# Performance work log

Hardware: AMD Instinct MI355X
Metric: run time of the kernel (lower is better)

## Reference

```python
import jax, jax.numpy as jnp
import numpy as np
from jax import lax


def setup_inputs() -> dict:
    key = jax.random.key(0)
    x = jax.random.normal(key, (8, 1, 2048, 2048), dtype=jnp.float32)
    return {"x": x}


def reference(x):
    # torch.median over the whole tensor returns the LOWER median for even counts:
    # k-th smallest element with k = (n - 1) // 2.
    n = x.size
    med = jnp.sort(x.ravel())[(n - 1) // 2]

    # Threshold everything <= median to zero.
    thr = jnp.where(x > med, x, jnp.zeros_like(x))

    # 7x7 max pool, stride 1, padding 3 (torch pads with -inf), output same HxW.
    maxed = lax.reduce_window(
        thr,
        -jnp.inf,
        lax.max,
        window_dimensions=(1, 1, 7, 7),
        window_strides=(1, 1, 1, 1),
        padding=((0, 0), (0, 0), (3, 3), (3, 3)),
    )

    # Keep only local maxima (entries equal to their window max), scaled by score.
    out = jnp.where(thr == maxed, thr, jnp.zeros_like(thr))
    return out
```

## Files before the change

kernel.cpp:

```cpp
#include <hip/hip_runtime.h>
#include <math.h>

#define IMG_H 2048
#define IMG_W 2048
#define TX 64
#define TY 64
#define HALO 3
#define IN_W (TX + 2 * HALO)
#define IN_H (TY + 2 * HALO)
#define SIN_STRIDE 71
#define SHM_STRIDE 65
#define CAND_CAP (1u << 20)
#define CBUF 1024

__device__ __forceinline__ unsigned f2key(unsigned u) {
    unsigned mask = (unsigned)(((int)u >> 31)) | 0x80000000u;
    return u ^ mask;
}
static inline unsigned f2key_host(float f) {
    union { float f; unsigned u; } c; c.f = f;
    unsigned mask = (unsigned)(((int)c.u >> 31)) | 0x80000000u;
    return c.u ^ mask;
}

__device__ __forceinline__ unsigned block_exscan(unsigned val, unsigned* tmp) {
    const int t = threadIdx.x;
    tmp[t] = val;
    __syncthreads();
#pragma unroll
    for (int off = 1; off < 256; off <<= 1) {
        unsigned v = (t >= off) ? tmp[t - off] : 0u;
        __syncthreads();
        tmp[t] += v;
        __syncthreads();
    }
    return tmp[t] - val;
}

template <int C>
__device__ __forceinline__ void find_crossing(const unsigned* bins, unsigned k,
                                              unsigned* tmp, unsigned* res) {
    unsigned s = 0;
#pragma unroll
    for (int j = 0; j < C; ++j) s += bins[threadIdx.x * C + j];
    unsigned ex = block_exscan(s, tmp);
    if (k >= ex && k < ex + s) {
        unsigned cum = ex;
        int b = threadIdx.x * C;
        while (cum + bins[b] <= k) { cum += bins[b]; ++b; }
        res[0] = (unsigned)b;
        res[1] = k - cum;
    }
    __syncthreads();
}

__global__ __launch_bounds__(256) void hist_window_kernel(
        const float4* __restrict__ x, int n4, unsigned* __restrict__ ghist,
        unsigned* __restrict__ ctrl, unsigned* __restrict__ candA,
        unsigned keyLo, unsigned keyHi) {
    __shared__ unsigned h[4 * 2048];
    __shared__ unsigned cbuf[CBUF];
    __shared__ unsigned ccnt, sbase, scnt;
    const int wave = threadIdx.x >> 6;
    unsigned* hw = &h[wave * 2048];
    for (int i = threadIdx.x; i < 4 * 2048; i += 256) h[i] = 0;
    if (threadIdx.x == 0) ccnt = 0;
    __syncthreads();
    const int stride = gridDim.x * blockDim.x;
    for (int i = blockIdx.x * blockDim.x + threadIdx.x; i < n4; i += stride) {
        float4 v = x[i];
        unsigned k0 = f2key(__float_as_uint(v.x));
        unsigned k1 = f2key(__float_as_uint(v.y));
        unsigned k2 = f2key(__float_as_uint(v.z));
        unsigned k3 = f2key(__float_as_uint(v.w));
        atomicAdd(&hw[k0 >> 21], 1u);
        atomicAdd(&hw[k1 >> 21], 1u);
        atomicAdd(&hw[k2 >> 21], 1u);
        atomicAdd(&hw[k3 >> 21], 1u);
        if (k0 > keyLo && k0 < keyHi) { unsigned p = atomicAdd(&ccnt, 1u); if (p < CBUF) cbuf[p] = k0; }
        if (k1 > keyLo && k1 < keyHi) { unsigned p = atomicAdd(&ccnt, 1u); if (p < CBUF) cbuf[p] = k1; }
        if (k2 > keyLo && k2 < keyHi) { unsigned p = atomicAdd(&ccnt, 1u); if (p < CBUF) cbuf[p] = k2; }
        if (k3 > keyLo && k3 < keyHi) { unsigned p = atomicAdd(&ccnt, 1u); if (p < CBUF) cbuf[p] = k3; }
    }
    __syncthreads();
    for (int b = threadIdx.x; b < 2048; b += 256) {
        unsigned s = h[b] + h[2048 + b] + h[4096 + b] + h[6144 + b];
        if (s) atomicAdd(&ghist[b], s);
    }
    if (threadIdx.x == 0) {
        unsigned c = ccnt;
        if (c > CBUF) { c = CBUF; atomicOr(&ctrl[3], 1u); }
        unsigned base = atomicAdd(&ctrl[2], c);
        if (base + c > CAND_CAP) {
            atomicOr(&ctrl[3], 1u);
            c = base < CAND_CAP ? CAND_CAP - base : 0;
        }
        sbase = base; scnt = c;
    }
    __syncthreads();
    for (unsigned i = threadIdx.x; i < scnt; i += 256) candA[sbase + i] = cbuf[i];
}

__global__ __launch_bounds__(256) void find_bucket_kernel(
        const unsigned* __restrict__ ghist, unsigned k, unsigned* __restrict__ ctrl,
        unsigned keyLo, unsigned keyHi) {
    __shared__ unsigned lh[2048];
    __shared__ unsigned tmp[256];
    __shared__ unsigned res[2];
    for (int i = threadIdx.x; i < 2048; i += 256) lh[i] = ghist[i];
    __syncthreads();
    find_crossing<8>(lh, k, tmp, res);
    if (threadIdx.x == 0) {
        unsigned b = res[0];
        ctrl[0] = b;
        ctrl[1] = res[1];
        unsigned lo = b << 21, hi = (b << 21) + 0x1FFFFFu;
        ctrl[4] = (lo > keyLo && hi < keyHi && ctrl[3] == 0u) ? 1u : 0u;
    }
}

__global__ __launch_bounds__(256) void compact_fallback_kernel(
        const float4* __restrict__ x, int n4, unsigned* __restrict__ ctrl,
        unsigned* __restrict__ candB) {
    if (ctrl[4]) return;
    const unsigned bucket = ctrl[0];
    const int stride = gridDim.x * blockDim.x;
    for (int i = blockIdx.x * blockDim.x + threadIdx.x; i < n4; i += stride) {
        float4 v = x[i];
        unsigned ks[4] = { f2key(__float_as_uint(v.x)), f2key(__float_as_uint(v.y)),
                           f2key(__float_as_uint(v.z)), f2key(__float_as_uint(v.w)) };
#pragma unroll
        for (int j = 0; j < 4; ++j)
            if ((ks[j] >> 21) == bucket) {
                unsigned p = atomicAdd(&ctrl[5], 1u);
                if (p < CAND_CAP) candB[p] = ks[j];
            }
    }
}

__global__ __launch_bounds__(256) void bucket_filter_kernel(
        const unsigned* __restrict__ ctrl_c, unsigned* __restrict__ ctrl,
        const unsigned* __restrict__ candA, unsigned* __restrict__ candC) {
    if (!ctrl_c[4]) return;
    const unsigned bucket = ctrl_c[0];
    unsigned M = ctrl_c[2];
    if (M > CAND_CAP) M = CAND_CAP;
    const int stride = gridDim.x * blockDim.x;
    for (unsigned i = blockIdx.x * blockDim.x + threadIdx.x; i < M; i += stride) {
        unsigned key = candA[i];
        if ((key >> 21) == bucket) {
            unsigned p = atomicAdd(&ctrl[6], 1u);
            if (p < CAND_CAP) candC[p] = key;
        }
    }
}

__global__ __launch_bounds__(256) void final_select_kernel(
        unsigned* __restrict__ ctrl, const unsigned* __restrict__ candC,
        const unsigned* __restrict__ candB, float* __restrict__ medp) {
    __shared__ unsigned h2[2048];
    __shared__ unsigned tmp[256];
    __shared__ unsigned res[2];
    const unsigned covered = ctrl[4];
    const unsigned* src = covered ? candC : candB;
    unsigned M = covered ? ctrl[6] : ctrl[5];
    if (M > CAND_CAP) M = CAND_CAP;
    const unsigned bucket = ctrl[0];
    const unsigned r = ctrl[1];

    for (int i = threadIdx.x; i < 2048; i += 256) h2[i] = 0;
    __syncthreads();
    for (unsigned i = threadIdx.x; i < M; i += 256) {
        unsigned key = src[i];
        if ((key >> 21) == bucket) atomicAdd(&h2[(key >> 10) & 0x7FFu], 1u);
    }
    __syncthreads();
    find_crossing<8>(h2, r, tmp, res);
    const unsigned pref = (bucket << 11) | res[0];
    const unsigned r2 = res[1];
    __syncthreads();

    for (int i = threadIdx.x; i < 1024; i += 256) h2[i] = 0;
    __syncthreads();
    for (unsigned i = threadIdx.x; i < M; i += 256) {
        unsigned key = src[i];
        if ((key >> 10) == pref) atomicAdd(&h2[key & 0x3FFu], 1u);
    }
    __syncthreads();
    find_crossing<4>(h2, r2, tmp, res);
    if (threadIdx.x == 0) {
        unsigned key = (pref << 10) | res[0];
        unsigned u = (key & 0x80000000u) ? (key ^ 0x80000000u) : ~key;
        *medp = __uint_as_float(u);
    }
}

__global__ __launch_bounds__(256) void nms_kernel(const float* __restrict__ x,
                                                  float* __restrict__ out,
                                                  const float* __restrict__ medp) {
    __shared__ float sin_[IN_H * SIN_STRIDE];
    __shared__ float shm[IN_H * SHM_STRIDE];
    const float med = *medp;
    const int tx0 = blockIdx.x * TX;
    const int ty0 = blockIdx.y * TY;
    const size_t ib = (size_t)blockIdx.z * (size_t)(IMG_H * IMG_W);
    const float* img = x + ib;
    float* oimg = out + ib;

    for (int i = threadIdx.x; i < IN_H * IN_W; i += 256) {
        int rr = i / IN_W;
        int cc = i - rr * IN_W;
        int gy = ty0 + rr - HALO;
        int gx = tx0 + cc - HALO;
        float v = -INFINITY;
        if ((unsigned)gy < (unsigned)IMG_H && (unsigned)gx < (unsigned)IMG_W) {
            float xv = img[(size_t)gy * IMG_W + gx];
            v = (xv > med) ? xv : 0.0f;
        }
        sin_[rr * SIN_STRIDE + cc] = v;
    }
    __syncthreads();

    for (int task = threadIdx.x; task < IN_H * 4; task += 256) {
        int rr = task >> 2;
        int s = task & 3;
        int c0 = s * 16;
        const float* p = &sin_[rr * SIN_STRIDE + c0];
        float v[22];
#pragma unroll
        for (int j = 0; j < 22; ++j) v[j] = p[j];
        float m2[21];
#pragma unroll
        for (int j = 0; j < 21; ++j) m2[j] = fmaxf(v[j], v[j + 1]);
        float m4[19];
#pragma unroll
        for (int j = 0; j < 19; ++j) m4[j] = fmaxf(m2[j], m2[j + 2]);
        float* q = &shm[rr * SHM_STRIDE + c0];
#pragma unroll
        for (int j = 0; j < 16; ++j) q[j] = fmaxf(m4[j], m4[j + 3]);
    }
    __syncthreads();

    {
        int col = threadIdx.x & 63;
        int seg = threadIdx.x >> 6;
        int r0 = seg * 16;
        float v[22];
#pragma unroll
        for (int j = 0; j < 22; ++j) v[j] = shm[(r0 + j) * SHM_STRIDE + col];
        float m2[21];
#pragma unroll
        for (int j = 0; j < 21; ++j) m2[j] = fmaxf(v[j], v[j + 1]);
        float m4[19];
#pragma unroll
        for (int j = 0; j < 19; ++j) m4[j] = fmaxf(m2[j], m2[j + 2]);
#pragma unroll
        for (int j = 0; j < 16; ++j) {
            float m = fmaxf(m4[j], m4[j + 3]);
            float t = sin_[(r0 + j + HALO) * SIN_STRIDE + col + HALO];
            oimg[(size_t)(ty0 + r0 + j) * IMG_W + (tx0 + col)] = (t == m) ? t : 0.0f;
        }
    }
}

extern "C" void kernel_launch(void* const* d_in, const int* in_sizes, int n_in,
                              void* d_out, int out_size, void* d_ws, size_t ws_size,
                              hipStream_t stream) {
    const float* x = (const float*)d_in[0];
    float* out = (float*)d_out;
    const int n = in_sizes[0];
    const int n4 = n / 4;
    const unsigned k = (unsigned)((n - 1) / 2);

    unsigned char* ws = (unsigned char*)d_ws;
    unsigned* ghist = (unsigned*)ws;
    unsigned* ctrl = (unsigned*)(ws + 2048 * 4);
    float* medp = (float*)(ctrl + 7);
    unsigned* candA = (unsigned*)(ws + 2048 * 4 + 64);
    unsigned* candB = candA + CAND_CAP;
    unsigned* candC = candB + CAND_CAP;
    const size_t reserved = 2048 * 4 + 64;

    hipMemsetAsync(d_ws, 0, reserved, stream);

    const float W = 0.002f;
    const unsigned keyLo = f2key_host(-W);
    const unsigned keyHi = f2key_host(W);

    hist_window_kernel<<<1024, 256, 0, stream>>>((const float4*)x, n4, ghist, ctrl, candA, keyLo, keyHi);
    find_bucket_kernel<<<1, 256, 0, stream>>>(ghist, k, ctrl, keyLo, keyHi);
    compact_fallback_kernel<<<1024, 256, 0, stream>>>((const float4*)x, n4, ctrl, candB);
    bucket_filter_kernel<<<64, 256, 0, stream>>>(ctrl, ctrl, candA, candC);
    final_select_kernel<<<1, 256, 0, stream>>>(ctrl, candC, candB, medp);

    dim3 grid(IMG_W / TX, IMG_H / TY, n / (IMG_H * IMG_W));
    nms_kernel<<<grid, 256, 0, stream>>>(x, out, medp);
}
```

Measured before the change: 330.9 us.

## Vectorize NMS tile loads/stores with float4 and shrink tile height to 32

Rewrites the max-pool/NMS kernel to load the haloed input tile with aligned float4 global reads and store outputs as float4. Tile height drops from 64 to 32 and the vertical pass now gives each thread 2 rows by 4 columns instead of 16 rows by 1 column. Shared strides are padded to multiples of 4 for 16-byte alignment, and a launch-bounds occupancy hint is added. This aims to cut global memory instructions in the memory-bound NMS stage, at the cost of more halo overhead per tile (38/32 rows vs 70/64) and possible shared-memory bank conflicts with the new strides.

After: 311.7 us, median of 2. 1.06x faster.

```diff
diff --git a/kernel.cpp b/kernel.cpp
--- a/kernel.cpp
+++ b/kernel.cpp
@@ -4,14 +4,17 @@
 #define IMG_H 2048
 #define IMG_W 2048
 #define TX 64
-#define TY 64
+#define TY 32
 #define HALO 3
-#define IN_W (TX + 2 * HALO)
-#define IN_H (TY + 2 * HALO)
-#define SIN_STRIDE 71
-#define SHM_STRIDE 65
+#define TILE_H (TY + 2 * HALO)
+#define SIN_STR 76
+#define SHM_STR 68
 #define CAND_CAP (1u << 20)
 #define CBUF 1024
+
+__device__ __forceinline__ float4 fmax4(float4 a, float4 b) {
+    return make_float4(fmaxf(a.x, b.x), fmaxf(a.y, b.y), fmaxf(a.z, b.z), fmaxf(a.w, b.w));
+}
 
 __device__ __forceinline__ unsigned f2key(unsigned u) {
     unsigned mask = (unsigned)(((int)u >> 31)) | 0x80000000u;
@@ -195,71 +198,100 @@
     }
 }
 
-__global__ __launch_bounds__(256) void nms_kernel(const float* __restrict__ x,
-                                                  float* __restrict__ out,
-                                                  const float* __restrict__ medp) {
-    __shared__ float sin_[IN_H * SIN_STRIDE];
-    __shared__ float shm[IN_H * SHM_STRIDE];
+__global__ __launch_bounds__(256, 6) void nms_kernel(const float* __restrict__ x,
+                                                     float* __restrict__ out,
+                                                     const float* __restrict__ medp) {
+    __shared__ __align__(16) float sin_[TILE_H * SIN_STR];
+    __shared__ __align__(16) float shm[TILE_H * SHM_STR];
     const float med = *medp;
     const int tx0 = blockIdx.x * TX;
     const int ty0 = blockIdx.y * TY;
     const size_t ib = (size_t)blockIdx.z * (size_t)(IMG_H * IMG_W);
     const float* img = x + ib;
     float* oimg = out + ib;
-
-    for (int i = threadIdx.x; i < IN_H * IN_W; i += 256) {
-        int rr = i / IN_W;
-        int cc = i - rr * IN_W;
+    const bool colsafe = (tx0 >= 4) && (tx0 + 68 <= IMG_W);
+
+    for (int task = threadIdx.x; task < TILE_H * 18; task += 256) {
+        int rr = task / 18;
+        int c4 = task - rr * 18;
         int gy = ty0 + rr - HALO;
-        int gx = tx0 + cc - HALO;
-        float v = -INFINITY;
-        if ((unsigned)gy < (unsigned)IMG_H && (unsigned)gx < (unsigned)IMG_W) {
-            float xv = img[(size_t)gy * IMG_W + gx];
-            v = (xv > med) ? xv : 0.0f;
+        int gx0 = tx0 - 4 + c4 * 4;
+        float4 v;
+        if ((unsigned)gy < (unsigned)IMG_H) {
+            if (colsafe) {
+                v = *(const float4*)(img + (size_t)gy * IMG_W + gx0);
+                v.x = (v.x > med) ? v.x : 0.0f;
+                v.y = (v.y > med) ? v.y : 0.0f;
+                v.z = (v.z > med) ? v.z : 0.0f;
+                v.w = (v.w > med) ? v.w : 0.0f;
+            } else {
+                float c[4];
+#pragma unroll
+                for (int j = 0; j < 4; ++j) {
+                    int gx = gx0 + j;
+                    if ((unsigned)gx < (unsigned)IMG_W) {
+                        float xv = img[(size_t)gy * IMG_W + gx];
+                        c[j] = (xv > med) ? xv : 0.0f;
+                    } else c[j] = -INFINITY;
+                }
+                v = make_float4(c[0], c[1], c[2], c[3]);
+            }
+        } else {
+            v = make_float4(-INFINITY, -INFINITY, -INFINITY, -INFINITY);
         }
-        sin_[rr * SIN_STRIDE + cc] = v;
-    }
-    __syncthreads();
-
-    for (int task = threadIdx.x; task < IN_H * 4; task += 256) {
+        *(float4*)&sin_[rr * SIN_STR + c4 * 4] = v;
+    }
+    __syncthreads();
+
+    for (int task = threadIdx.x; task < TILE_H * 4; task += 256) {
         int rr = task >> 2;
         int s = task & 3;
         int c0 = s * 16;
-        const float* p = &sin_[rr * SIN_STRIDE + c0];
-        float v[22];
-#pragma unroll
-        for (int j = 0; j < 22; ++j) v[j] = p[j];
-        float m2[21];
-#pragma unroll
-        for (int j = 0; j < 21; ++j) m2[j] = fmaxf(v[j], v[j + 1]);
-        float m4[19];
-#pragma unroll
-        for (int j = 0; j < 19; ++j) m4[j] = fmaxf(m2[j], m2[j + 2]);
-        float* q = &shm[rr * SHM_STRIDE + c0];
-#pragma unroll
-        for (int j = 0; j < 16; ++j) q[j] = fmaxf(m4[j], m4[j + 3]);
+        const float* p = &sin_[rr * SIN_STR + c0];
+        float v[24];
+#pragma unroll
+        for (int b = 0; b < 6; ++b) {
+            float4 q = *(const float4*)(p + 4 * b);
+            v[4 * b] = q.x; v[4 * b + 1] = q.y; v[4 * b + 2] = q.z; v[4 * b + 3] = q.w;
+        }
+        float m2[22];
+#pragma unroll
+        for (int j = 1; j <= 21; ++j) m2[j] = fmaxf(v[j], v[j + 1]);
+        float m4[20];
+#pragma unroll
+        for (int j = 1; j <= 19; ++j) m4[j] = fmaxf(m2[j], m2[j + 2]);
+        float o[16];
+#pragma unroll
+        for (int j = 0; j < 16; ++j) o[j] = fmaxf(m4[j + 1], m4[j + 4]);
+        float* q = &shm[rr * SHM_STR + c0];
+#pragma unroll
+        for (int b = 0; b < 4; ++b)
+            *(float4*)(q + 4 * b) = make_float4(o[4 * b], o[4 * b + 1], o[4 * b + 2], o[4 * b + 3]);
     }
     __syncthreads();
 
     {
-        int col = threadIdx.x & 63;
-        int seg = threadIdx.x >> 6;
-        int r0 = seg * 16;
-        float v[22];
-#pragma unroll
-        for (int j = 0; j < 22; ++j) v[j] = shm[(r0 + j) * SHM_STRIDE + col];
-        float m2[21];
-#pragma unroll
-        for (int j = 0; j < 21; ++j) m2[j] = fmaxf(v[j], v[j + 1]);
-        float m4[19];
-#pragma unroll
-        for (int j = 0; j < 19; ++j) m4[j] = fmaxf(m2[j], m2[j + 2]);
-#pragma unroll
-        for (int j = 0; j < 16; ++j) {
-            float m = fmaxf(m4[j], m4[j + 3]);
-            float t = sin_[(r0 + j + HALO) * SIN_STRIDE + col + HALO];
-            oimg[(size_t)(ty0 + r0 + j) * IMG_W + (tx0 + col)] = (t == m) ? t : 0.0f;
-        }
+        const int col4 = threadIdx.x & 15;
+        const int r0 = (threadIdx.x >> 4) * 2;
+        float4 v[8];
+#pragma unroll
+        for (int j = 0; j < 8; ++j) v[j] = *(const float4*)&shm[(r0 + j) * SHM_STR + col4 * 4];
+        float4 m2[7];
+#pragma unroll
+        for (int j = 0; j < 7; ++j) m2[j] = fmax4(v[j], v[j + 1]);
+        float4 m4[5];
+#pragma unroll
+        for (int j = 0; j < 5; ++j) m4[j] = fmax4(m2[j], m2[j + 2]);
+        float4 ma = fmax4(m4[0], m4[3]);
+        float4 mb = fmax4(m4[1], m4[4]);
+        float4 ta = *(const float4*)&sin_[(r0 + HALO) * SIN_STR + col4 * 4 + 4];
+        float4 tb = *(const float4*)&sin_[(r0 + 1 + HALO) * SIN_STR + col4 * 4 + 4];
+        float4 oa = make_float4((ta.x == ma.x) ? ta.x : 0.0f, (ta.y == ma.y) ? ta.y : 0.0f,
+                                (ta.z == ma.z) ? ta.z : 0.0f, (ta.w == ma.w) ? ta.w : 0.0f);
+        float4 ob = make_float4((tb.x == mb.x) ? tb.x : 0.0f, (tb.y == mb.y) ? tb.y : 0.0f,
+                                (tb.z == mb.z) ? tb.z : 0.0f, (tb.w == mb.w) ? tb.w : 0.0f);
+        *(float4*)(oimg + (size_t)(ty0 + r0) * IMG_W + tx0 + col4 * 4) = oa;
+        *(float4*)(oimg + (size_t)(ty0 + r0 + 1) * IMG_W + tx0 + col4 * 4) = ob;
     }
 }
 
```
